# Kernel optimization log

Hardware: AMD Instinct MI355X
Metric: run time of the kernel (lower is better)

The kernel has to match this reference:

```python
import jax, jax.numpy as jnp
import numpy as np

SCALE = 30.0  # self.s


def setup_inputs() -> dict:
    key = jax.random.key(0)
    x = jax.random.normal(key, (2048, 8, 128), dtype=jnp.float32)
    return {"x": x}


def reference(x):
    # x: [S, G, d] = [stepsize (speakers), gsize (utts/speaker), embed dim]
    S, G, d = x.shape
    # F.normalize(x, p=2, dim=2)
    xn = x / jnp.clip(jnp.linalg.norm(x, axis=2, keepdims=True), 1e-12)
    centroids = xn.mean(axis=1)  # [S, d]
    # exclusive centroids: mean over the G-1 other utterances, for every ii at once
    exc = (xn.sum(axis=1, keepdims=True) - xn) / (G - 1)  # [S, G, d]
    exc_n = exc / jnp.clip(jnp.linalg.norm(exc, axis=2, keepdims=True), 1e-8)
    # xn rows are unit norm, so cosine_similarity = dot with normalized exc
    cosine_exc = jnp.sum(xn * exc_n, axis=2)  # [S, G]
    # NOTE: in the source, one_hot = zeros then scatter_(0) stays all-zero, so the
    # ArcFace phi branch contributes nothing: output == cosine_exc exactly.
    cent_n = centroids / jnp.clip(jnp.linalg.norm(centroids, axis=1, keepdims=True), 1e-8)
    # full similarity of every utterance against every centroid: [S, G, S]
    cos_sim = SCALE * jnp.einsum('sgd,td->sgt', xn, cent_n)
    # replace diagonal (own-speaker entry) with exclusive-centroid similarity
    diag = jnp.arange(S)
    cos_sim = cos_sim.at[diag, :, diag].set(SCALE * cosine_exc)
    # torch.clamp(cos_sim, 1e-06) clamps min only
    logits = jnp.clip(cos_sim, 1e-6).reshape(S * G, S)
    labels = jnp.repeat(jnp.arange(S), G)  # repeat_interleave(arange(S), G)
    logp = jax.nn.log_softmax(logits, axis=-1)
    nloss = -jnp.mean(logp[jnp.arange(S * G), labels])
    return nloss
```

## Files before the change

### kernel.cpp

```cpp
#include <hip/hip_runtime.h>
#include <hip/hip_bf16.h>

#define S_DIM 2048
#define G_DIM 8
#define D_DIM 128
#define N_ROWS (S_DIM * G_DIM)
#define SCALE 30.0f
#define NSPLIT 16
#define TCHUNK (S_DIM / NSPLIT)
#define NCOMBINE 64

typedef __attribute__((ext_vector_type(8))) short bf16x8;
typedef __attribute__((ext_vector_type(4))) float f32x4;

__device__ __forceinline__ float wave_allreduce_sum(float v) {
    #pragma unroll
    for (int m = 32; m >= 1; m >>= 1) v += __shfl_xor(v, m, 64);
    return v;
}

__global__ __launch_bounds__(512) void prep_kernel(
    const float* __restrict__ x,
    __hip_bfloat16* __restrict__ xnb,
    __hip_bfloat16* __restrict__ centb,
    float* __restrict__ cosexc,
    float* __restrict__ acc_out,
    unsigned int* __restrict__ counter)
{
    __shared__ float xs[G_DIM][D_DIM];
    __shared__ float csum[D_DIM];

    const int s    = blockIdx.x;
    const int g    = threadIdx.x >> 6;
    const int lane = threadIdx.x & 63;
    const int d0 = lane, d1 = lane + 64;

    if (s == 0 && threadIdx.x == 0) { acc_out[0] = 0.0f; counter[0] = 0u; }

    const float* xr = x + (s * G_DIM + g) * D_DIM;
    float a0 = xr[d0], a1 = xr[d1];

    float ss  = wave_allreduce_sum(a0 * a0 + a1 * a1);
    float inv = 1.0f / fmaxf(sqrtf(ss), 1e-12f);
    float x0 = a0 * inv, x1 = a1 * inv;

    xs[g][d0] = x0;
    xs[g][d1] = x1;
    __hip_bfloat16* xw = xnb + (s * G_DIM + g) * D_DIM;
    xw[d0] = __float2bfloat16(x0);
    xw[d1] = __float2bfloat16(x1);
    __syncthreads();

    if (threadIdx.x < D_DIM) {
        float c = 0.0f;
        #pragma unroll
        for (int gg = 0; gg < G_DIM; ++gg) c += xs[gg][threadIdx.x];
        csum[threadIdx.x] = c;
    }
    __syncthreads();

    float e0 = (csum[d0] - x0) * (1.0f / (G_DIM - 1));
    float e1 = (csum[d1] - x1) * (1.0f / (G_DIM - 1));
    float ess = wave_allreduce_sum(e0 * e0 + e1 * e1);
    float ed  = fmaxf(sqrtf(ess), 1e-8f);
    float dot = wave_allreduce_sum(x0 * e0 + x1 * e1);
    if (lane == 0) cosexc[s * G_DIM + g] = dot / ed;

    if (g == 0) {
        float c0 = csum[d0], c1 = csum[d1];
        float css  = wave_allreduce_sum(c0 * c0 + c1 * c1);
        float cnrm = sqrtf(css) * (1.0f / G_DIM);
        float scl  = (1.0f / G_DIM) / fmaxf(cnrm, 1e-8f);
        centb[s * D_DIM + d0] = __float2bfloat16(c0 * scl);
        centb[s * D_DIM + d1] = __float2bfloat16(c1 * scl);
    }
}

__global__ __launch_bounds__(256, 4) void score_kernel(
    const __hip_bfloat16* __restrict__ xnb,
    const __hip_bfloat16* __restrict__ centb,
    const float* __restrict__ cosexc,
    float* __restrict__ psum,
    float* __restrict__ plab)
{
    const int wave  = threadIdx.x >> 6;
    const int lane  = threadIdx.x & 63;
    const int row0  = (blockIdx.x * 4 + wave) * 64;
    const int split = blockIdx.y;
    const int tbase = split * TCHUNK;
    const int nIdx  = lane & 15;
    const int quad  = lane >> 4;
    const int s0    = row0 >> 3;

    const short* xsrc = (const short*)xnb;
    bf16x8 afrag[4][4];
    #pragma unroll
    for (int m = 0; m < 4; ++m) {
        const int abase = (row0 + m * 16 + nIdx) * D_DIM + quad * 8;
        #pragma unroll
        for (int kc = 0; kc < 4; ++kc)
            afrag[m][kc] = *(const bf16x8*)(xsrc + abase + kc * 32);
    }

    float sumexp[4][4];
    #pragma unroll
    for (int m = 0; m < 4; ++m)
        #pragma unroll
        for (int r = 0; r < 4; ++r) sumexp[m][r] = 0.0f;

    const short* csrc = (const short*)centb;
    for (int t0 = tbase; t0 < tbase + TCHUNK; t0 += 16) {
        bf16x8 bfrag[4];
        const int bbase = (t0 + nIdx) * D_DIM + quad * 8;
        #pragma unroll
        for (int kc = 0; kc < 4; ++kc)
            bfrag[kc] = *(const bf16x8*)(csrc + bbase + kc * 32);

        f32x4 acc[4];
        #pragma unroll
        for (int m = 0; m < 4; ++m) acc[m] = (f32x4){0.f, 0.f, 0.f, 0.f};
        #pragma unroll
        for (int kc = 0; kc < 4; ++kc)
            #pragma unroll
            for (int m = 0; m < 4; ++m)
                acc[m] = __builtin_amdgcn_mfma_f32_16x16x32_bf16(
                    afrag[m][kc], bfrag[kc], acc[m], 0, 0, 0);

        const int t = t0 + nIdx;
        if (t0 <= s0 + 7 && t0 + 16 > s0) {
            #pragma unroll
            for (int m = 0; m < 4; ++m) {
                #pragma unroll
                for (int r = 0; r < 4; ++r) {
                    const int grow = row0 + m * 16 + quad * 4 + r;
                    float l = fmaxf(SCALE * acc[m][r], 1e-6f);
                    if (t == (grow >> 3)) {
                        l = fmaxf(SCALE * cosexc[grow], 1e-6f);
                        plab[grow] = l;
                    }
                    sumexp[m][r] += __expf(l - SCALE);
                }
            }
        } else {
            #pragma unroll
            for (int m = 0; m < 4; ++m) {
                #pragma unroll
                for (int r = 0; r < 4; ++r) {
                    float l = fmaxf(SCALE * acc[m][r], 1e-6f);
                    sumexp[m][r] += __expf(l - SCALE);
                }
            }
        }
    }

    #pragma unroll
    for (int m = 0; m < 4; ++m) {
        #pragma unroll
        for (int r = 0; r < 4; ++r) {
            #pragma unroll
            for (int msk = 1; msk <= 8; msk <<= 1)
                sumexp[m][r] += __shfl_xor(sumexp[m][r], msk, 64);
        }
    }
    if (nIdx == 0) {
        #pragma unroll
        for (int m = 0; m < 4; ++m)
            #pragma unroll
            for (int r = 0; r < 4; ++r)
                psum[split * N_ROWS + row0 + m * 16 + quad * 4 + r] = sumexp[m][r];
    }
}

__global__ __launch_bounds__(256) void combine_kernel(
    const float* __restrict__ psum, const float* __restrict__ plab,
    float* __restrict__ acc_out, unsigned int* __restrict__ counter,
    float* __restrict__ out)
{
    __shared__ float red[4];
    const int row = blockIdx.x * 256 + threadIdx.x;

    float s = 0.0f;
    #pragma unroll
    for (int j = 0; j < NSPLIT; ++j) s += psum[j * N_ROWS + row];
    float loss = SCALE + logf(s) - plab[row];

    float v = wave_allreduce_sum(loss);
    const int wave = threadIdx.x >> 6;
    if ((threadIdx.x & 63) == 0) red[wave] = v;
    __syncthreads();
    if (threadIdx.x == 0) {
        atomicAdd(acc_out, red[0] + red[1] + red[2] + red[3]);
        __threadfence();
        unsigned int prev = atomicAdd(counter, 1u);
        if (prev == NCOMBINE - 1) {
            float total = atomicAdd(acc_out, 0.0f);
            out[0] = total * (1.0f / N_ROWS);
        }
    }
}

extern "C" void kernel_launch(void* const* d_in, const int* in_sizes, int n_in,
                              void* d_out, int out_size, void* d_ws, size_t ws_size,
                              hipStream_t stream) {
    const float* x = (const float*)d_in[0];
    char* ws = (char*)d_ws;

    size_t off = 0;
    __hip_bfloat16* xnb   = (__hip_bfloat16*)(ws + off); off += (size_t)N_ROWS * D_DIM * 2;
    __hip_bfloat16* centb = (__hip_bfloat16*)(ws + off); off += (size_t)S_DIM * D_DIM * 2;
    float* cosexc = (float*)(ws + off); off += (size_t)N_ROWS * 4;
    float* psum   = (float*)(ws + off); off += (size_t)NSPLIT * N_ROWS * 4;
    float* plab   = (float*)(ws + off); off += (size_t)N_ROWS * 4;
    float* acc    = (float*)(ws + off); off += 4;
    unsigned int* counter = (unsigned int*)(ws + off); off += 4;
    float* out = (float*)d_out;

    prep_kernel<<<S_DIM, 512, 0, stream>>>(x, xnb, centb, cosexc, acc, counter);
    score_kernel<<<dim3(N_ROWS / 256, NSPLIT), 256, 0, stream>>>(xnb, centb, cosexc, psum, plab);
    combine_kernel<<<NCOMBINE, 256, 0, stream>>>(psum, plab, acc, counter, out);
}
```

Before: 93.06 us.

## Stage centroid tile in LDS via async global-to-LDS loads with swizzle

Each score block now loads its whole 128-row centroid chunk (32 KB) into shared memory up front with global_load_lds, using an XOR-like rotation swizzle to avoid bank conflicts. The inner loop then reads B fragments from LDS instead of re-reading global/L2 memory for every 16-row step in each wave. The off-diagonal logit path also folds scale, offset and clamp into a single fma plus max. The 32 KB of LDS per block may limit occupancy, and the swizzle has to match the global_load_lds per-wave layout exactly for the results to be correct.

```diff
diff --git a/kernel.cpp b/kernel.cpp
--- a/kernel.cpp
+++ b/kernel.cpp
@@ -83,8 +83,11 @@
     float* __restrict__ psum,
     float* __restrict__ plab)
 {
+    __shared__ short bsm[TCHUNK * D_DIM];
+
     const int wave  = threadIdx.x >> 6;
     const int lane  = threadIdx.x & 63;
+    const int tid   = threadIdx.x;
     const int row0  = (blockIdx.x * 4 + wave) * 64;
     const int split = blockIdx.y;
     const int tbase = split * TCHUNK;
@@ -92,6 +95,23 @@
     const int quad  = lane >> 4;
     const int s0    = row0 >> 3;
 
+    {
+        const short* gsrc = (const short*)centb;
+        #pragma unroll
+        for (int j = 0; j < 8; ++j) {
+            const int s  = j * 256 + tid;
+            const int r  = s >> 4;
+            const int cc = s & 15;
+            const int c  = (cc - r) & 15;
+            const short* g = gsrc + (size_t)(tbase + r) * D_DIM + c * 8;
+            __builtin_amdgcn_global_load_lds(
+                (const __attribute__((address_space(1))) void*)g,
+                (__attribute__((address_space(3))) void*)
+                    ((char*)bsm + j * 4096 + wave * 1024),
+                16, 0, 0);
+        }
+    }
+
     const short* xsrc = (const short*)xnb;
     bf16x8 afrag[4][4];
     #pragma unroll
@@ -108,13 +128,16 @@
         #pragma unroll
         for (int r = 0; r < 4; ++r) sumexp[m][r] = 0.0f;
 
-    const short* csrc = (const short*)centb;
+    __syncthreads();
+
     for (int t0 = tbase; t0 < tbase + TCHUNK; t0 += 16) {
+        const int lr = (t0 - tbase) + nIdx;
         bf16x8 bfrag[4];
-        const int bbase = (t0 + nIdx) * D_DIM + quad * 8;
-        #pragma unroll
-        for (int kc = 0; kc < 4; ++kc)
-            bfrag[kc] = *(const bf16x8*)(csrc + bbase + kc * 32);
+        #pragma unroll
+        for (int kc = 0; kc < 4; ++kc) {
+            const int cc = (quad + kc * 4 + lr) & 15;
+            bfrag[kc] = *(const bf16x8*)(bsm + lr * D_DIM + cc * 8);
+        }
 
         f32x4 acc[4];
         #pragma unroll
@@ -146,8 +169,8 @@
             for (int m = 0; m < 4; ++m) {
                 #pragma unroll
                 for (int r = 0; r < 4; ++r) {
-                    float l = fmaxf(SCALE * acc[m][r], 1e-6f);
-                    sumexp[m][r] += __expf(l - SCALE);
+                    float e = fmaxf(fmaf(SCALE, acc[m][r], -SCALE), 1e-6f - SCALE);
+                    sumexp[m][r] += __expf(e);
                 }
             }
         }
```

Result: faster. 83.12 us (-10.7%).
